# Kernel tuning notes

Measured on AMD Instinct MI355X. Metric: run time of the kernel, lower is better.

The kernel has to match this reference:

```python
import jax, jax.numpy as jnp
import numpy as np

D_MODEL = 1024
NUM_HEADS = 16
DEPTH = D_MODEL // NUM_HEADS


def setup_inputs() -> dict:
    key = jax.random.key(0)
    ks = jax.random.split(key, 9)
    B, S = 2, 2048
    scale = 1.0 / np.sqrt(D_MODEL)
    x = jax.random.normal(ks[0], (B, S, D_MODEL), dtype=jnp.float32)
    wq = jax.random.normal(ks[1], (D_MODEL, D_MODEL), dtype=jnp.float32) * scale
    bq = jax.random.normal(ks[2], (D_MODEL,), dtype=jnp.float32) * 0.01
    wk = jax.random.normal(ks[3], (D_MODEL, D_MODEL), dtype=jnp.float32) * scale
    bk = jax.random.normal(ks[4], (D_MODEL,), dtype=jnp.float32) * 0.01
    wv = jax.random.normal(ks[5], (D_MODEL, D_MODEL), dtype=jnp.float32) * scale
    bv = jax.random.normal(ks[6], (D_MODEL,), dtype=jnp.float32) * 0.01
    wo = jax.random.normal(ks[7], (D_MODEL, D_MODEL), dtype=jnp.float32) * scale
    bo = jax.random.normal(ks[8], (D_MODEL,), dtype=jnp.float32) * 0.01
    return {"x": x, "wq": wq, "bq": bq, "wk": wk, "bk": bk,
            "wv": wv, "bv": bv, "wo": wo, "bo": bo}


def reference(x, wq, bq, wk, bk, wv, bv, wo, bo):
    B, S, _ = x.shape
    def split_heads(t):  # [B,S,D] -> [B,H,S,depth]
        return t.reshape(B, S, NUM_HEADS, DEPTH).transpose(0, 2, 1, 3)
    q = split_heads(x @ wq + bq)
    k = split_heads(x @ wk + bk)
    v = split_heads(x @ wv + bv)
    # scaled dot-product attention, full [B,H,S,S] scores as in the original
    logits = jnp.einsum('bhqd,bhkd->bhqk', q, k) / jnp.sqrt(
        jnp.asarray(DEPTH, dtype=jnp.float32))
    attn = jax.nn.softmax(logits, axis=-1)
    out = jnp.einsum('bhqk,bhkd->bhqd', attn, v)
    out = out.transpose(0, 2, 1, 3).reshape(B, S, D_MODEL)
    return out @ wo + bo
```

## Files before the change

kernel.cpp:

```cpp
#include <hip/hip_runtime.h>


#define S_LEN 2048
#define DM 1024
#define QSCALE 0.1803368801111244f

typedef unsigned short u16;
typedef unsigned int u32;
typedef __attribute__((ext_vector_type(8))) short short8;
typedef __attribute__((ext_vector_type(4))) float f32x4;
typedef __attribute__((ext_vector_type(4))) unsigned short u16x4;
typedef __attribute__((ext_vector_type(2))) unsigned int u32x2;

__device__ inline u16 f2bf(float f) {
    u32 u = __float_as_uint(f);
    u = u + 0x7fffu + ((u >> 16) & 1u);
    return (u16)(u >> 16);
}
__device__ inline void gld_lds16(const u16* g, u16* l) {
    __builtin_amdgcn_global_load_lds(
        (const __attribute__((address_space(1))) void*)g,
        (__attribute__((address_space(3))) void*)l, 16, 0, 0);
}
__device__ inline f32x4 mfma16(short8 a, short8 b, f32x4 c) {
    return __builtin_amdgcn_mfma_f32_16x16x32_bf16(a, b, c, 0, 0, 0);
}

__global__ void prep_all(const float* __restrict__ x, u16* __restrict__ xb,
                         const float* __restrict__ wq, const float* __restrict__ wk,
                         const float* __restrict__ wv, const float* __restrict__ wo,
                         const float* __restrict__ bq, const float* __restrict__ bk,
                         const float* __restrict__ bv, const float* __restrict__ bo,
                         u16* __restrict__ wallT, u16* __restrict__ woT,
                         float* __restrict__ biasAll, float* __restrict__ biasO) {
    const int t = threadIdx.x;
    if (blockIdx.x < 2048) {
        const size_t i8 = ((size_t)blockIdx.x * 256 + t) * 8;
        const f32x4 a = ((const f32x4*)x)[i8 / 4];
        const f32x4 b = ((const f32x4*)x)[i8 / 4 + 1];
        u16 o[8];
#pragma unroll
        for (int i = 0; i < 4; i++) { o[i] = f2bf(a[i]); o[4 + i] = f2bf(b[i]); }
        *(short8*)(xb + i8) = *(const short8*)o;
        return;
    }
    const int bid = blockIdx.x - 2048;
    if (bid == 1024) {
#pragma unroll
        for (int i = 0; i < 4; i++) {
            const int idx = i * 256 + t;
            biasAll[idx]        = bq[idx] * QSCALE;
            biasAll[1024 + idx] = bk[idx];
            biasAll[2048 + idx] = bv[idx];
            biasO[idx]          = bo[idx];
        }
        return;
    }
    __shared__ float lds[64][65];
    const int m  = bid >> 8;
    const int tk = (bid >> 4) & 15;
    const int tn = bid & 15;
    const float* src = (m == 0) ? wq : (m == 1) ? wk : (m == 2) ? wv : wo;
    const float scale = (m == 0) ? QSCALE : 1.0f;
    const int r4 = t >> 6, c = t & 63;
#pragma unroll
    for (int i = 0; i < 16; i++) {
        const int k = tk * 64 + i * 4 + r4;
        lds[i * 4 + r4][c] = src[(size_t)k * 1024 + tn * 64 + c];
    }
    __syncthreads();
#pragma unroll
    for (int i = 0; i < 16; i++) {
        const int n = tn * 64 + i * 4 + r4;
        const int k = tk * 64 + c;
        const u16 v = f2bf(lds[c][i * 4 + r4] * scale);
        if (m < 3) wallT[((size_t)m * 1024 + n) * 1024 + k] = v;
        else       woT[(size_t)n * 1024 + k] = v;
    }
}

__global__ __launch_bounds__(512, 2)
void gemm_qkv(const u16* __restrict__ A, const u16* __restrict__ Bt,
              const float* __restrict__ bias, u16* __restrict__ Cq,
              u16* __restrict__ Ck, u16* __restrict__ Cv,
              const int K, const int N) {
    __shared__ __align__(16) u16 smem[65536];
    u16* const As0 = smem;
    u16* const As1 = smem + 16384;
    u16* const Bs0 = smem + 32768;
    u16* const Bs1 = smem + 49152;

    const int tid = threadIdx.x;
    const int w = tid >> 6, lane = tid & 63;
    const int wr = w >> 2, wc = w & 3;
    const int l16 = lane & 15, quad = lane >> 4;
    const int tm = blockIdx.x * 256;
    const int tn = blockIdx.y * 256;

    const int swzcol = ((lane & 7) ^ (lane >> 3)) * 8;
    const u16* agA = A  + (size_t)(tm + w * 32 + (lane >> 3)) * K + swzcol;
    const u16* bgB = Bt + (size_t)(tn + w * 32 + (lane >> 3)) * K + swzcol;

    const int xr = l16 & 7;
    const int aOff = (wr * 128 + l16) * 64;
    const int bOff = (wc * 64 + l16) * 64;
    const int sk0 = (quad ^ xr) * 8;
    const int sk1 = ((4 | quad) ^ xr) * 8;

    f32x4 acc[8][4];
#pragma unroll
    for (int i = 0; i < 8; i++)
#pragma unroll
        for (int j = 0; j < 4; j++) acc[i][j] = (f32x4){0.f, 0.f, 0.f, 0.f};

#pragma unroll
    for (int i = 0; i < 4; i++) {
        gld_lds16(agA + i * 8 * K, As0 + w * 2048 + i * 512);
        gld_lds16(bgB + i * 8 * K, Bs0 + w * 2048 + i * 512);
    }
    __syncthreads();

    auto tile = [&](int t, const u16* Ac, const u16* Bc,
                    u16* sAw, u16* sBw, bool pf) {
        const int kb1 = (t + 1) * 64;
        short8 a0[4], a1[4], a2[4], a3[4], b0[4], b1[4];
        if (pf) {
            gld_lds16(agA + kb1,          sAw + w * 2048);
            gld_lds16(agA + 8 * K + kb1,  sAw + w * 2048 + 512);
            gld_lds16(bgB + kb1,          sBw + w * 2048);
        }
#pragma unroll
        for (int j = 0; j < 4; j++) b0[j] = *(const short8*)(Bc + bOff + j * 1024 + sk0);
#pragma unroll
        for (int i = 0; i < 4; i++) a0[i] = *(const short8*)(Ac + aOff + i * 1024 + sk0);
        __builtin_amdgcn_s_barrier();
        asm volatile("s_waitcnt lgkmcnt(0)" ::: "memory");
        __builtin_amdgcn_sched_barrier(0);
        __builtin_amdgcn_s_setprio(1);
#pragma unroll
        for (int i = 0; i < 4; i++)
#pragma unroll
            for (int j = 0; j < 4; j++)
                acc[i][j] = mfma16(a0[i], b0[j], acc[i][j]);
        __builtin_amdgcn_s_setprio(0);
        __builtin_amdgcn_sched_barrier(0);
        __builtin_amdgcn_s_barrier();
        if (pf) {
            gld_lds16(agA + 16 * K + kb1, sAw + w * 2048 + 1024);
            gld_lds16(agA + 24 * K + kb1, sAw + w * 2048 + 1536);
            gld_lds16(bgB + 8 * K + kb1,  sBw + w * 2048 + 512);
        }
#pragma unroll
        for (int i = 0; i < 4; i++) a1[i] = *(const short8*)(Ac + aOff + (4 + i) * 1024 + sk0);
        __builtin_amdgcn_s_barrier();
        asm volatile("s_waitcnt lgkmcnt(0)" ::: "memory");
        __builtin_amdgcn_sched_barrier(0);
        __builtin_amdgcn_s_setprio(1);
#pragma unroll
        for (int i = 0; i < 4; i++)
#pragma unroll
            for (int j = 0; j < 4; j++)
                acc[4 + i][j] = mfma16(a1[i], b0[j], acc[4 + i][j]);
        __builtin_amdgcn_s_setprio(0);
        __builtin_amdgcn_sched_barrier(0);
        __builtin_amdgcn_s_barrier();
        if (pf) {
            gld_lds16(bgB + 16 * K + kb1, sBw + w * 2048 + 1024);
            gld_lds16(bgB + 24 * K + kb1, sBw + w * 2048 + 1536);
        }
#pragma unroll
        for (int j = 0; j < 4; j++) b1[j] = *(const short8*)(Bc + bOff + j * 1024 + sk1);
#pragma unroll
        for (int i = 0; i < 4; i++) a2[i] = *(const short8*)(Ac + aOff + i * 1024 + sk1);
        __builtin_amdgcn_s_barrier();
        asm volatile("s_waitcnt lgkmcnt(0)" ::: "memory");
        __builtin_amdgcn_sched_barrier(0);
        __builtin_amdgcn_s_setprio(1);
#pragma unroll
        for (int i = 0; i < 4; i++)
#pragma unroll
            for (int j = 0; j < 4; j++)
                acc[i][j] = mfma16(a2[i], b1[j], acc[i][j]);
        __builtin_amdgcn_s_setprio(0);
        __builtin_amdgcn_sched_barrier(0);
        __builtin_amdgcn_s_barrier();
#pragma unroll
        for (int i = 0; i < 4; i++) a3[i] = *(const short8*)(Ac + aOff + (4 + i) * 1024 + sk1);
        __builtin_amdgcn_s_barrier();
        asm volatile("s_waitcnt lgkmcnt(0)" ::: "memory");
        __builtin_amdgcn_sched_barrier(0);
        __builtin_amdgcn_s_setprio(1);
#pragma unroll
        for (int i = 0; i < 4; i++)
#pragma unroll
            for (int j = 0; j < 4; j++)
                acc[4 + i][j] = mfma16(a3[i], b1[j], acc[4 + i][j]);
        __builtin_amdgcn_s_setprio(0);
        asm volatile("s_waitcnt vmcnt(0)" ::: "memory");
        __builtin_amdgcn_sched_barrier(0);
        __builtin_amdgcn_s_barrier();
    };

#pragma unroll 1
    for (int tp = 0; tp < 8; tp++) {
        tile(2 * tp,     As0, Bs0, As1, Bs1, true);
        tile(2 * tp + 1, As1, Bs1, As0, Bs0, tp < 7);
    }

    __syncthreads();
    u16* const Ct = smem;
    const int wnL = wc & 1;
#pragma unroll 1
    for (int q = 0; q < 4; q++) {
        const int qi = q >> 1, qj = q & 1;
        const int tmq = tm + qi * 128;
        const int tnq = tn + qj * 128;
        const int region = tnq >> 10;
        if (wr == qi && (wc >> 1) == qj) {
            if (region < 2) {
#pragma unroll
                for (int j = 0; j < 4; j++) {
                    const int colL = wnL * 64 + j * 16 + l16;
                    const float bv = bias[tnq + colL];
#pragma unroll
                    for (int i = 0; i < 8; i++) {
                        const int row0 = i * 16 + quad * 4;
#pragma unroll
                        for (int r = 0; r < 4; r++)
                            Ct[(row0 + r) * 136 + colL] = f2bf(acc[i][j][r] + bv);
                    }
                }
            } else {
#pragma unroll
                for (int j = 0; j < 4; j++) {
                    const int colL = wnL * 64 + j * 16 + l16;
                    const float bv = bias[tnq + colL];
#pragma unroll
                    for (int i = 0; i < 8; i++) {
                        const int row0 = i * 16 + quad * 4;
                        u16x4 pk;
#pragma unroll
                        for (int r = 0; r < 4; r++) pk[r] = f2bf(acc[i][j][r] + bv);
                        *(u16x4*)(Ct + colL * 132 + row0) = pk;
                    }
                }
            }
        }
        __syncthreads();
        if (region == 0) {
#pragma unroll
            for (int p = 0; p < 4; p++) {
                const int rowL = p * 32 + (tid >> 4);
                const int c8 = (tid & 15) * 8;
                const short8 v = *(const short8*)(Ct + rowL * 136 + c8);
                *(short8*)(Cq + (size_t)(tmq + rowL) * 1024 + tnq + c8) = v;
            }
        } else if (region == 1) {
            const int b = tmq >> 11, sBase = tmq & 2047;
#pragma unroll
            for (int p = 0; p < 4; p++) {
                const int rowL = p * 32 + (tid >> 4);
                const int c8 = (tid & 15) * 8;
                const short8 v = *(const short8*)(Ct + rowL * 136 + c8);
                const int s = sBase + rowL;
                const int hd = (tnq - 1024) + c8;
                const int h = hd >> 6, dd = hd & 63;
                const int chunk = ((dd >> 3) + s) & 7;
                *(short8*)(Ck + (((size_t)(b * 16 + h) * 2048 + s) << 6) + chunk * 8) = v;
            }
        } else {
            const int b = tmq >> 11, tBase = (tmq & 2047) >> 6;
            const int hBase = (tnq >> 6) - 32;
#pragma unroll
            for (int p = 0; p < 4; p++) {
                const int cid = p * 512 + tid;
                const int q3 = cid & 7;
                const int colL = (cid >> 3) & 127;
                const int half = cid >> 10;
                const int d = colL & 63;
                const int h = hBase + (colL >> 6);
                const int c = (q3 - d) & 7;
                const int base = (c & 3) * 4 + ((c & 4) << 3);
                const u32x2 Ar = *(const u32x2*)(Ct + colL * 132 + half * 64 + base);
                const u32x2 Br = *(const u32x2*)(Ct + colL * 132 + half * 64 + base + 16);
                union { u32 u[4]; short8 s8; } o;
                o.u[0] = __builtin_amdgcn_perm(Br[0], Ar[0], 0x05040100u);
                o.u[1] = __builtin_amdgcn_perm(Br[0], Ar[0], 0x07060302u);
                o.u[2] = __builtin_amdgcn_perm(Br[1], Ar[1], 0x05040100u);
                o.u[3] = __builtin_amdgcn_perm(Br[1], Ar[1], 0x07060302u);
                *(short8*)(Cv + (((size_t)((b * 16 + h) * 32 + tBase + half)) << 12) +
                           d * 64 + q3 * 8) = o.s8;
            }
        }
        __syncthreads();
    }
}

__global__ __launch_bounds__(256, 2)
void gemm_out64(const u16* __restrict__ A, const u16* __restrict__ Bt,
                const float* __restrict__ bias, float* __restrict__ C,
                const int K, const int N) {
    __shared__ __align__(16) u16 As[64 * 32];
    __shared__ __align__(16) u16 Bs[128 * 32];
    const int tid = threadIdx.x;
    const int w = tid >> 6, lane = tid & 63;
    const int wm = w >> 1, wn = w & 1;
    const int l16 = lane & 15, quad = lane >> 4;
    const int tm = blockIdx.x * 64;
    const int tn = blockIdx.y * 128;

    const int sr = w * 16 + (lane >> 2);
    const int sc = (lane & 3) * 8;
    const u16* ag  = A + (size_t)(tm + sr) * K + sc;
    const u16* bg0 = Bt + (size_t)(tn + sr) * K + sc;
    const u16* bg1 = Bt + (size_t)(tn + sr + 64) * K + sc;
    u16* al = As + w * 512;
    u16* bl = Bs + w * 512;

    f32x4 acc[2][4];
#pragma unroll
    for (int i = 0; i < 2; i++)
#pragma unroll
        for (int j = 0; j < 4; j++) acc[i][j] = (f32x4){0.f, 0.f, 0.f, 0.f};

    for (int kb = 0; kb < K; kb += 32) {
        __syncthreads();
        gld_lds16(ag + kb, al);
        gld_lds16(bg0 + kb, bl);
        gld_lds16(bg1 + kb, bl + 2048);
        __syncthreads();
        short8 af[2], bfr[4];
#pragma unroll
        for (int i = 0; i < 2; i++)
            af[i] = *(const short8*)(As + (wm * 32 + i * 16 + l16) * 32 + quad * 8);
#pragma unroll
        for (int j = 0; j < 4; j++)
            bfr[j] = *(const short8*)(Bs + (wn * 64 + j * 16 + l16) * 32 + quad * 8);
#pragma unroll
        for (int i = 0; i < 2; i++)
#pragma unroll
            for (int j = 0; j < 4; j++)
                acc[i][j] = mfma16(af[i], bfr[j], acc[i][j]);
    }
#pragma unroll
    for (int j = 0; j < 4; j++) {
        const int col = tn + wn * 64 + j * 16 + l16;
        const float bv = bias[col];
#pragma unroll
        for (int i = 0; i < 2; i++) {
            const int row0 = tm + wm * 32 + i * 16 + quad * 4;
#pragma unroll
            for (int r = 0; r < 4; r++)
                C[(size_t)(row0 + r) * N + col] = acc[i][j][r] + bv;
        }
    }
}

__global__ __launch_bounds__(256, 2)
void flash_attn(const u16* __restrict__ Qb, const u16* __restrict__ Ktg,
                const u16* __restrict__ Vtb, u16* __restrict__ O) {
    __shared__ __align__(16) u16 Ks[2][8192];
    __shared__ __align__(16) u16 Vs[2][8192];
    const int tid = threadIdx.x;
    const int w = tid >> 6, lane = tid & 63;
    const int l16 = lane & 15, quad = lane >> 4;
    const int lid = blockIdx.x + blockIdx.y * 16;
    const int bh = lid & 31, b = bh >> 4, h = bh & 15;
    const int q0 = (lid >> 5) * 128 + w * 32;

    short8 qf[2][2];
#pragma unroll
    for (int u = 0; u < 2; u++) {
        const size_t qrow = (size_t)(b * S_LEN + q0 + u * 16 + l16) * 1024 + h * 64;
        qf[u][0] = *(const short8*)(Qb + qrow + quad * 8);
        qf[u][1] = *(const short8*)(Qb + qrow + 32 + quad * 8);
    }
    u16 ones_s[8];
#pragma unroll
    for (int i = 0; i < 8; i++) ones_s[i] = 0x3F80u;
    const short8 ones = *(const short8*)ones_s;

    const u16* kg = Ktg + ((size_t)bh << 17) + w * 2048 + lane * 8;
    const u16* vg = Vtb + ((size_t)bh << 17) + w * 2048 + lane * 8;
    u16* kl0 = &Ks[0][0] + w * 2048;
    u16* vl0 = &Vs[0][0] + w * 2048;
    u16* kl1 = &Ks[1][0] + w * 2048;
    u16* vl1 = &Vs[1][0] + w * 2048;

    const int ka0 = l16 * 64 + ((quad + l16) & 7) * 8;
    const int ka1 = l16 * 64 + ((4 + quad + l16) & 7) * 8;

    f32x4 o[2][4], osum[2];
#pragma unroll
    for (int u = 0; u < 2; u++) {
        osum[u] = (f32x4){0.f, 0.f, 0.f, 0.f};
#pragma unroll
        for (int d = 0; d < 4; d++) o[u][d] = (f32x4){0.f, 0.f, 0.f, 0.f};
    }
    const f32x4 zz = (f32x4){0.f, 0.f, 0.f, 0.f};

#pragma unroll
    for (int k = 0; k < 4; k++) {
        gld_lds16(kg + k * 512, kl0 + k * 512);
        gld_lds16(vg + k * 512, vl0 + k * 512);
    }
    __syncthreads();

    auto step = [&](int t, const u16* Kc, const u16* Vc,
                    u16* klN, u16* vlN, bool pf) {
        if (pf) {
            const int off = (t + 1) * 8192;
#pragma unroll
            for (int k = 0; k < 4; k++) {
                gld_lds16(kg + off + k * 512, klN + k * 512);
                gld_lds16(vg + off + k * 512, vlN + k * 512);
            }
            asm volatile("s_waitcnt vmcnt(8)" ::: "memory");
        } else {
            asm volatile("s_waitcnt vmcnt(0)" ::: "memory");
        }
        __builtin_amdgcn_s_barrier();

        f32x4 s[2][8];
        __builtin_amdgcn_s_setprio(1);
#pragma unroll
        for (int a = 0; a < 8; a++) {
            const short8 kf0 = *(const short8*)(Kc + a * 1024 + ka0);
            const short8 kf1 = *(const short8*)(Kc + a * 1024 + ka1);
#pragma unroll
            for (int u = 0; u < 2; u++) {
                s[u][a] = mfma16(kf0, qf[u][0], zz);
                s[u][a] = mfma16(kf1, qf[u][1], s[u][a]);
            }
        }
        __builtin_amdgcn_s_setprio(0);
        union { u32 u[4]; short8 s8; } pu[2][4];
#pragma unroll
        for (int u = 0; u < 2; u++) {
#pragma unroll
            for (int p = 0; p < 4; p++) {
#pragma unroll
                for (int r = 0; r < 4; r++) {
                    const float e0 = __builtin_amdgcn_exp2f(s[u][2 * p][r]);
                    const float e1 = __builtin_amdgcn_exp2f(s[u][2 * p + 1][r]);
                    pu[u][p].u[r] = __builtin_amdgcn_perm(
                        __float_as_uint(e1), __float_as_uint(e0), 0x07060302u);
                }
                osum[u] = mfma16(ones, pu[u][p].s8, osum[u]);
            }
        }
        __builtin_amdgcn_s_setprio(1);
#pragma unroll
        for (int dv = 0; dv < 4; dv++) {
            const short8 vf0a = *(const short8*)(Vc + dv * 1024 + ka0);
            const short8 vf1a = *(const short8*)(Vc + dv * 1024 + ka1);
            const short8 vf0b = *(const short8*)(Vc + 4096 + dv * 1024 + ka0);
            const short8 vf1b = *(const short8*)(Vc + 4096 + dv * 1024 + ka1);
#pragma unroll
            for (int u = 0; u < 2; u++) {
                o[u][dv] = mfma16(vf0a, pu[u][0].s8, o[u][dv]);
                o[u][dv] = mfma16(vf1a, pu[u][1].s8, o[u][dv]);
                o[u][dv] = mfma16(vf0b, pu[u][2].s8, o[u][dv]);
                o[u][dv] = mfma16(vf1b, pu[u][3].s8, o[u][dv]);
            }
        }
        __builtin_amdgcn_s_setprio(0);
        __builtin_amdgcn_s_barrier();
    };

#pragma unroll 1
    for (int tp = 0; tp < S_LEN / 256; tp++) {
        step(2 * tp,     &Ks[0][0], &Vs[0][0], kl1, vl1, true);
        step(2 * tp + 1, &Ks[1][0], &Vs[1][0], kl0, vl0, tp < S_LEN / 256 - 1);
    }

#pragma unroll
    for (int u = 0; u < 2; u++) {
        const float inv = 1.0f / osum[u][0];
        const size_t obase =
            (size_t)(b * S_LEN + q0 + u * 16 + l16) * DM + h * 64 + quad * 4;
#pragma unroll
        for (int d = 0; d < 4; d++) {
            u16x4 pk;
#pragma unroll
            for (int r = 0; r < 4; r++) pk[r] = f2bf(o[u][d][r] * inv);
            *(u16x4*)(O + obase + d * 16) = pk;
        }
    }
}

extern "C" void kernel_launch(void* const* d_in, const int* in_sizes, int n_in,
                              void* d_out, int out_size, void* d_ws, size_t ws_size,
                              hipStream_t stream) {
    const float* x  = (const float*)d_in[0];
    const float* wq = (const float*)d_in[1];
    const float* bq = (const float*)d_in[2];
    const float* wk = (const float*)d_in[3];
    const float* bk = (const float*)d_in[4];
    const float* wv = (const float*)d_in[5];
    const float* bv = (const float*)d_in[6];
    const float* wo = (const float*)d_in[7];
    const float* bo = (const float*)d_in[8];

    char* ws = (char*)d_ws;
    u16*   wallT   = (u16*)(ws + 64);
    u16*   woT     = (u16*)(ws + 6291520);
    float* biasAll = (float*)(ws + 8388672);
    float* biasO   = (float*)(ws + 8400960);
    u16*   xb      = (u16*)(ws + 8405056);
    u16*   Qb      = (u16*)(ws + 16793664);
    u16*   Ktg     = (u16*)(ws + 25182272);
    u16*   Vtb     = (u16*)(ws + 33570880);
    u16*   Obuf    = (u16*)(ws + 41959488);

    prep_all<<<3073, 256, 0, stream>>>(x, xb, wq, wk, wv, wo, bq, bk, bv, bo,
                                       wallT, woT, biasAll, biasO);
    gemm_qkv<<<dim3(16, 12), 512, 0, stream>>>(xb, wallT, biasAll,
                                               Qb, Ktg, Vtb, 1024, 3072);
    flash_attn<<<dim3(16, 32), 256, 0, stream>>>(Qb, Ktg, Vtb, Obuf);
    gemm_out64<<<dim3(64, 8), 256, 0, stream>>>(Obuf, woT, biasO,
                                                (float*)d_out, 1024, 1024);
}
```

Baseline: 186.0 us.

## Restructure QKV GEMM into four-slot K=32 LDS ring with deeper prefetch

```diff
diff --git a/kernel.cpp b/kernel.cpp
--- a/kernel.cpp
+++ b/kernel.cpp
@@ -3,6 +3,7 @@
 
 #define S_LEN 2048
 #define DM 1024
+#define KQ 1024
 #define QSCALE 0.1803368801111244f
 
 typedef unsigned short u16;
@@ -24,6 +25,11 @@
 }
 __device__ inline f32x4 mfma16(short8 a, short8 b, f32x4 c) {
     return __builtin_amdgcn_mfma_f32_16x16x32_bf16(a, b, c, 0, 0, 0);
+}
+template<int N> __device__ __forceinline__ void vmwait() {
+    if constexpr (N == 8)      asm volatile("s_waitcnt vmcnt(8)" ::: "memory");
+    else if constexpr (N == 4) asm volatile("s_waitcnt vmcnt(4)" ::: "memory");
+    else if constexpr (N == 0) asm volatile("s_waitcnt vmcnt(0)" ::: "memory");
 }
 
 __global__ void prep_all(const float* __restrict__ x, u16* __restrict__ xb,
@@ -79,33 +85,105 @@
     }
 }
 
+__device__ __forceinline__ void qkv_mfma16x(f32x4 (&acc)[8][4], const short8* a,
+                                            const short8* b, const int ibase) {
+    __builtin_amdgcn_s_setprio(1);
+#pragma unroll
+    for (int i = 0; i < 4; i++)
+#pragma unroll
+        for (int j = 0; j < 4; j++)
+            acc[ibase + i][j] = mfma16(a[i], b[j], acc[ibase + i][j]);
+    __builtin_amdgcn_s_setprio(0);
+}
+
+template<int VM1, int VM3, bool ST01, bool ST23>
+__device__ __forceinline__ void qkv_tile(
+    const u16* rA0, const u16* rA1, const u16* rB0, const u16* rB1,
+    u16* dA3, u16* dB3, u16* dA4, u16* dB4,
+    const u16* gA3, const u16* gB3, const u16* gA4, const u16* gB4,
+    const int w, const int aRd, const int bRd, f32x4 (&acc)[8][4]) {
+    short8 a0[4], a1[4], a2[4], a3[4], b0[4], b1[4];
+    if (ST01) { gld_lds16(gA3, dA3 + w * 1024);
+                gld_lds16(gA3 + 16 * KQ, dA3 + w * 1024 + 512); }
+#pragma unroll
+    for (int j = 0; j < 4; j++) b0[j] = *(const short8*)(rB0 + bRd + j * 512);
+#pragma unroll
+    for (int i = 0; i < 4; i++) a0[i] = *(const short8*)(rA0 + aRd + i * 512);
+    __builtin_amdgcn_s_barrier();
+    asm volatile("s_waitcnt lgkmcnt(0)" ::: "memory");
+    __builtin_amdgcn_sched_barrier(0);
+    qkv_mfma16x(acc, a0, b0, 0);
+    __builtin_amdgcn_sched_barrier(0);
+    __builtin_amdgcn_s_barrier();
+    if (ST01) { gld_lds16(gB3, dB3 + w * 1024);
+                gld_lds16(gB3 + 16 * KQ, dB3 + w * 1024 + 512); }
+#pragma unroll
+    for (int i = 0; i < 4; i++) a1[i] = *(const short8*)(rA0 + aRd + 2048 + i * 512);
+    __builtin_amdgcn_s_barrier();
+    asm volatile("s_waitcnt lgkmcnt(0)" ::: "memory");
+    __builtin_amdgcn_sched_barrier(0);
+    qkv_mfma16x(acc, a1, b0, 4);
+    vmwait<VM1>();
+    __builtin_amdgcn_sched_barrier(0);
+    __builtin_amdgcn_s_barrier();
+    if (ST23) { gld_lds16(gA4, dA4 + w * 1024);
+                gld_lds16(gA4 + 16 * KQ, dA4 + w * 1024 + 512); }
+#pragma unroll
+    for (int j = 0; j < 4; j++) b1[j] = *(const short8*)(rB1 + bRd + j * 512);
+#pragma unroll
+    for (int i = 0; i < 4; i++) a2[i] = *(const short8*)(rA1 + aRd + i * 512);
+    __builtin_amdgcn_s_barrier();
+    asm volatile("s_waitcnt lgkmcnt(0)" ::: "memory");
+    __builtin_amdgcn_sched_barrier(0);
+    qkv_mfma16x(acc, a2, b1, 0);
+    __builtin_amdgcn_sched_barrier(0);
+    __builtin_amdgcn_s_barrier();
+    if (ST23) { gld_lds16(gB4, dB4 + w * 1024);
+                gld_lds16(gB4 + 16 * KQ, dB4 + w * 1024 + 512); }
+#pragma unroll
+    for (int i = 0; i < 4; i++) a3[i] = *(const short8*)(rA1 + aRd + 2048 + i * 512);
+    __builtin_amdgcn_s_barrier();
+    asm volatile("s_waitcnt lgkmcnt(0)" ::: "memory");
+    __builtin_amdgcn_sched_barrier(0);
+    qkv_mfma16x(acc, a3, b1, 4);
+    vmwait<VM3>();
+    __builtin_amdgcn_sched_barrier(0);
+    __builtin_amdgcn_s_barrier();
+}
+
 __global__ __launch_bounds__(512, 2)
 void gemm_qkv(const u16* __restrict__ A, const u16* __restrict__ Bt,
               const float* __restrict__ bias, u16* __restrict__ Cq,
               u16* __restrict__ Ck, u16* __restrict__ Cv,
               const int K, const int N) {
     __shared__ __align__(16) u16 smem[65536];
-    u16* const As0 = smem;
-    u16* const As1 = smem + 16384;
-    u16* const Bs0 = smem + 32768;
-    u16* const Bs1 = smem + 49152;
+    u16* const Asl0 = smem;
+    u16* const Asl1 = smem + 8192;
+    u16* const Asl2 = smem + 16384;
+    u16* const Asl3 = smem + 24576;
+    u16* const Bsl0 = smem + 32768;
+    u16* const Bsl1 = smem + 40960;
+    u16* const Bsl2 = smem + 49152;
+    u16* const Bsl3 = smem + 57344;
 
     const int tid = threadIdx.x;
     const int w = tid >> 6, lane = tid & 63;
     const int wr = w >> 2, wc = w & 3;
     const int l16 = lane & 15, quad = lane >> 4;
-    const int tm = blockIdx.x * 256;
-    const int tn = blockIdx.y * 256;
-
-    const int swzcol = ((lane & 7) ^ (lane >> 3)) * 8;
-    const u16* agA = A  + (size_t)(tm + w * 32 + (lane >> 3)) * K + swzcol;
-    const u16* bgB = Bt + (size_t)(tn + w * 32 + (lane >> 3)) * K + swzcol;
-
-    const int xr = l16 & 7;
-    const int aOff = (wr * 128 + l16) * 64;
-    const int bOff = (wc * 64 + l16) * 64;
-    const int sk0 = (quad ^ xr) * 8;
-    const int sk1 = ((4 | quad) ^ xr) * 8;
+
+    const int lid0 = blockIdx.x + (blockIdx.y << 4);
+    const int swz = (lid0 & 7) * 24 + (lid0 >> 3);
+    const int tm = (swz / 12) * 256;
+    const int tn = (swz % 12) * 256;
+
+    const u16* Ag = A  + (size_t)(tm + w * 32 + (lane >> 2)) * K
+                       + (((lane & 3) ^ ((lane >> 3) & 3)) * 8);
+    const u16* Bg = Bt + (size_t)(tn + w * 32 + (lane >> 2)) * K
+                       + (((lane & 3) ^ ((lane >> 3) & 3)) * 8);
+
+    const int xq = (quad ^ ((l16 >> 1) & 3)) * 8;
+    const int aRd = (wr * 128 + l16) * 32 + xq;
+    const int bRd = (wc * 64 + l16) * 32 + xq;
 
     f32x4 acc[8][4];
 #pragma unroll
@@ -113,99 +191,43 @@
 #pragma unroll
         for (int j = 0; j < 4; j++) acc[i][j] = (f32x4){0.f, 0.f, 0.f, 0.f};
 
-#pragma unroll
-    for (int i = 0; i < 4; i++) {
-        gld_lds16(agA + i * 8 * K, As0 + w * 2048 + i * 512);
-        gld_lds16(bgB + i * 8 * K, Bs0 + w * 2048 + i * 512);
-    }
-    __syncthreads();
-
-    auto tile = [&](int t, const u16* Ac, const u16* Bc,
-                    u16* sAw, u16* sBw, bool pf) {
-        const int kb1 = (t + 1) * 64;
-        short8 a0[4], a1[4], a2[4], a3[4], b0[4], b1[4];
-        if (pf) {
-            gld_lds16(agA + kb1,          sAw + w * 2048);
-            gld_lds16(agA + 8 * K + kb1,  sAw + w * 2048 + 512);
-            gld_lds16(bgB + kb1,          sBw + w * 2048);
-        }
-#pragma unroll
-        for (int j = 0; j < 4; j++) b0[j] = *(const short8*)(Bc + bOff + j * 1024 + sk0);
-#pragma unroll
-        for (int i = 0; i < 4; i++) a0[i] = *(const short8*)(Ac + aOff + i * 1024 + sk0);
-        __builtin_amdgcn_s_barrier();
-        asm volatile("s_waitcnt lgkmcnt(0)" ::: "memory");
-        __builtin_amdgcn_sched_barrier(0);
-        __builtin_amdgcn_s_setprio(1);
-#pragma unroll
-        for (int i = 0; i < 4; i++)
-#pragma unroll
-            for (int j = 0; j < 4; j++)
-                acc[i][j] = mfma16(a0[i], b0[j], acc[i][j]);
-        __builtin_amdgcn_s_setprio(0);
-        __builtin_amdgcn_sched_barrier(0);
-        __builtin_amdgcn_s_barrier();
-        if (pf) {
-            gld_lds16(agA + 16 * K + kb1, sAw + w * 2048 + 1024);
-            gld_lds16(agA + 24 * K + kb1, sAw + w * 2048 + 1536);
-            gld_lds16(bgB + 8 * K + kb1,  sBw + w * 2048 + 512);
-        }
-#pragma unroll
-        for (int i = 0; i < 4; i++) a1[i] = *(const short8*)(Ac + aOff + (4 + i) * 1024 + sk0);
-        __builtin_amdgcn_s_barrier();
-        asm volatile("s_waitcnt lgkmcnt(0)" ::: "memory");
-        __builtin_amdgcn_sched_barrier(0);
-        __builtin_amdgcn_s_setprio(1);
-#pragma unroll
-        for (int i = 0; i < 4; i++)
-#pragma unroll
-            for (int j = 0; j < 4; j++)
-                acc[4 + i][j] = mfma16(a1[i], b0[j], acc[4 + i][j]);
-        __builtin_amdgcn_s_setprio(0);
-        __builtin_amdgcn_sched_barrier(0);
-        __builtin_amdgcn_s_barrier();
-        if (pf) {
-            gld_lds16(bgB + 16 * K + kb1, sBw + w * 2048 + 1024);
-            gld_lds16(bgB + 24 * K + kb1, sBw + w * 2048 + 1536);
-        }
-#pragma unroll
-        for (int j = 0; j < 4; j++) b1[j] = *(const short8*)(Bc + bOff + j * 1024 + sk1);
-#pragma unroll
-        for (int i = 0; i < 4; i++) a2[i] = *(const short8*)(Ac + aOff + i * 1024 + sk1);
-        __builtin_amdgcn_s_barrier();
-        asm volatile("s_waitcnt lgkmcnt(0)" ::: "memory");
-        __builtin_amdgcn_sched_barrier(0);
-        __builtin_amdgcn_s_setprio(1);
-#pragma unroll
-        for (int i = 0; i < 4; i++)
-#pragma unroll
-            for (int j = 0; j < 4; j++)
-                acc[i][j] = mfma16(a2[i], b1[j], acc[i][j]);
-        __builtin_amdgcn_s_setprio(0);
-        __builtin_amdgcn_sched_barrier(0);
-        __builtin_amdgcn_s_barrier();
-#pragma unroll
-        for (int i = 0; i < 4; i++) a3[i] = *(const short8*)(Ac + aOff + (4 + i) * 1024 + sk1);
-        __builtin_amdgcn_s_barrier();
-        asm volatile("s_waitcnt lgkmcnt(0)" ::: "memory");
-        __builtin_amdgcn_sched_barrier(0);
-        __builtin_amdgcn_s_setprio(1);
-#pragma unroll
-        for (int i = 0; i < 4; i++)
-#pragma unroll
-            for (int j = 0; j < 4; j++)
-                acc[4 + i][j] = mfma16(a3[i], b1[j], acc[4 + i][j]);
-        __builtin_amdgcn_s_setprio(0);
-        asm volatile("s_waitcnt vmcnt(0)" ::: "memory");
-        __builtin_amdgcn_sched_barrier(0);
-        __builtin_amdgcn_s_barrier();
-    };
+    gld_lds16(Ag,            Asl0 + w * 1024);
+    gld_lds16(Ag + 16 * KQ,  Asl0 + w * 1024 + 512);
+    gld_lds16(Bg,            Bsl0 + w * 1024);
+    gld_lds16(Bg + 16 * KQ,  Bsl0 + w * 1024 + 512);
+    gld_lds16(Ag + 32,           Asl1 + w * 1024);
+    gld_lds16(Ag + 16 * KQ + 32, Asl1 + w * 1024 + 512);
+    gld_lds16(Bg + 32,           Bsl1 + w * 1024);
+    gld_lds16(Bg + 16 * KQ + 32, Bsl1 + w * 1024 + 512);
+    gld_lds16(Ag + 64,           Asl2 + w * 1024);
+    gld_lds16(Ag + 16 * KQ + 64, Asl2 + w * 1024 + 512);
+    gld_lds16(Bg + 64,           Bsl2 + w * 1024);
+    gld_lds16(Bg + 16 * KQ + 64, Bsl2 + w * 1024 + 512);
+    asm volatile("s_waitcnt vmcnt(8)" ::: "memory");
+    __builtin_amdgcn_s_barrier();
 
 #pragma unroll 1
-    for (int tp = 0; tp < 8; tp++) {
-        tile(2 * tp,     As0, Bs0, As1, Bs1, true);
-        tile(2 * tp + 1, As1, Bs1, As0, Bs0, tp < 7);
-    }
+    for (int tp = 0; tp < 7; tp++) {
+        const int h = tp * 128;
+        qkv_tile<8, 8, true, true>(Asl0, Asl1, Bsl0, Bsl1,
+                                   Asl3, Bsl3, Asl0, Bsl0,
+                                   Ag + h + 96,  Bg + h + 96,
+                                   Ag + h + 128, Bg + h + 128,
+                                   w, aRd, bRd, acc);
+        qkv_tile<8, 8, true, true>(Asl2, Asl3, Bsl2, Bsl3,
+                                   Asl1, Bsl1, Asl2, Bsl2,
+                                   Ag + h + 160, Bg + h + 160,
+                                   Ag + h + 192, Bg + h + 192,
+                                   w, aRd, bRd, acc);
+    }
+    qkv_tile<8, 4, true, false>(Asl0, Asl1, Bsl0, Bsl1,
+                                Asl3, Bsl3, Asl0, Bsl0,
+                                Ag + 992, Bg + 992, Ag, Bg,
+                                w, aRd, bRd, acc);
+    qkv_tile<0, -1, false, false>(Asl2, Asl3, Bsl2, Bsl3,
+                                  Asl1, Bsl1, Asl2, Bsl2,
+                                  Ag, Bg, Ag, Bg,
+                                  w, aRd, bRd, acc);
 
     __syncthreads();
     u16* const Ct = smem;
```

Result: no change. 185.5 us (-0.3%).
